# Kernel optimization log

Measured on AMD Instinct MI355X. Metric: run time of the kernel, lower is better.

## Reference

```python
import jax, jax.numpy as jnp
import numpy as np
from jax import lax

B, T, D, H, W = 2, 16, 64, 64, 64
E, HID, K = 4, 128, 3
NS = 0.01  # noise_scale
EPS = 1e-5  # LayerNorm eps (torch default)


def setup_inputs() -> dict:
    key = jax.random.key(0)
    ks = jax.random.split(key, 20)
    r = lambda i, shape, s=1.0: jax.random.normal(ks[i], shape, dtype=jnp.float32) * s
    return {
        "x_real": r(0, (B, T, D, H, W)),
        "x_imag": r(1, (B, T, D, H, W)),
        "dt": jax.random.uniform(ks[2], (B, T), dtype=jnp.float32, minval=0.1, maxval=1.0),
        "noise_eps_real": r(3, (B * H * W, T, D)),
        "noise_eps_imag": r(4, (B * H * W, T, D)),
        "ln_s_w": jnp.ones((2 * D,), jnp.float32),
        "ln_s_b": jnp.zeros((2 * D,), jnp.float32),
        "conv_w": r(5, (K, K, 2 * D, 2 * D), 0.02),  # HWIO
        "conv_b": jnp.zeros((2 * D,), jnp.float32),
        "ln_t_w": jnp.ones((2 * D,), jnp.float32),
        "ln_t_b": jnp.zeros((2 * D,), jnp.float32),
        "lam_re": r(6, (D,)),
        "lam_im": r(7, (D,)),
        "src_bias_re": r(8, (D,), 0.02),
        "src_bias_im": r(9, (D,), 0.02),
        "enc_re": r(10, (D, D), 0.125),
        "enc_im": r(11, (D, D), 0.125),
        "dec_re": r(12, (D, D), 0.125),
        "dec_im": r(13, (D, D), 0.125),
        "router_w": r(14, (2 * D, E), 0.02),
        "router_b": jnp.zeros((E,), jnp.float32),
        "w1": r(15, (E, 2 * D, HID), 0.02),
        "b1": jnp.zeros((E, HID), jnp.float32),
        "w2": r(16, (E, HID, 2 * D), 0.02),
        "b2": jnp.zeros((E, 2 * D), jnp.float32),
    }


def _complex_ln(zr, zi, w, b):
    # LayerNorm over concatenated [real, imag] last dim, then re-split to complex
    zc = jnp.concatenate([zr, zi], axis=-1)
    mu = jnp.mean(zc, -1, keepdims=True)
    var = jnp.var(zc, -1, keepdims=True)
    zn = (zc - mu) * lax.rsqrt(var + EPS) * w + b
    r, i = jnp.split(zn, 2, axis=-1)
    return r + 1j * i


def reference(x_real, x_imag, dt, noise_eps_real, noise_eps_imag,
              ln_s_w, ln_s_b, conv_w, conv_b, ln_t_w, ln_t_b,
              lam_re, lam_im, src_bias_re, src_bias_im,
              enc_re, enc_im, dec_re, dec_im,
              router_w, router_b, w1, b1, w2, b2):
    x = x_real + 1j * x_imag  # (B,T,D,H,W) complex
    resid = x
    # --- spatial: complex norm + clifford-style conv on stacked real/imag channels ---
    xs = jnp.transpose(x.reshape(B * T, D, H, W), (0, 2, 3, 1))  # (BT,H,W,D)
    zn = _complex_ln(xs.real, xs.imag, ln_s_w, ln_s_b)
    xc = jnp.concatenate([zn.real, zn.imag], axis=-1)  # (BT,H,W,2D)
    y = lax.conv_general_dilated(xc, conv_w, (1, 1), 'SAME',
                                 dimension_numbers=('NHWC', 'HWIO', 'NHWC')) + conv_b
    yr, yi = jnp.split(y, 2, axis=-1)
    x = jnp.transpose(yr + 1j * yi, (0, 3, 1, 2)).reshape(B, T, D, H, W) + resid
    resid = x
    # --- temporal: eigen-basis encode, decay-forced parallel scan, decode ---
    xt = jnp.transpose(x, (0, 3, 4, 1, 2)).reshape(B * H * W, T, D)
    xt = _complex_ln(xt.real, xt.imag, ln_t_w, ln_t_b)  # complex (N,T,D)
    dtE = jnp.broadcast_to(dt[:, None, None, :], (B, H, W, T)).reshape(B * H * W, T)
    lam = -jax.nn.softplus(lam_re) + 1j * lam_im  # stable per-mode eigenvalues (D,)
    a = jnp.exp(lam[None, None, :] * dtE[:, :, None])  # decay op (N,T,D)
    forcing = (a - 1.0) / lam  # ZOH forcing op
    Eb = enc_re + 1j * enc_im
    bias = src_bias_re + 1j * src_bias_im
    u = (jnp.einsum('ntd,de->nte', xt, Eb) + bias) * forcing
    u = u + NS * jnp.sqrt(dtE)[:, :, None] * (noise_eps_real + 1j * noise_eps_imag)

    def comb(c1, c2):  # first-order linear recurrence h_t = a_t h_{t-1} + u_t
        a1, b1_ = c1
        a2, b2_ = c2
        return a1 * a2, b1_ * a2 + b2_

    _, h = lax.associative_scan(comb, (a, u), axis=1)
    Db = dec_re + 1j * dec_im
    drift = jnp.einsum('nte,ed->ntd', h, Db).real  # (N,T,D)
    x = jnp.transpose(drift.reshape(B, H, W, T, D), (0, 3, 4, 1, 2)) + resid
    # --- MoE FFN on per-pixel tokens (real/imag concat) ---
    tc = jnp.transpose(x, (0, 1, 3, 4, 2))  # (B,T,H,W,D) complex
    tok = jnp.concatenate([tc.real, tc.imag], axis=-1).reshape(-1, 2 * D)  # (N2,2D)
    gates = jax.nn.softmax(tok @ router_w + router_b, axis=-1)  # (N2,E)
    hdn = jax.nn.gelu(jnp.einsum('nd,edh->neh', tok, w1) + b1)
    yo = jnp.einsum('neh,eho->neo', hdn, w2) + b2
    out = jnp.einsum('ne,neo->no', gates, yo)
    dr, di = jnp.split(out, 2, axis=-1)
    delta = jnp.transpose((dr + 1j * di).reshape(B, T, H, W, D), (0, 1, 4, 2, 3))
    x = x + delta
    return jnp.stack([x.real, x.imag], axis=0)  # (2,B,T,D,H,W)
```

## Files before the change

kernel.cpp:

```cpp
#include <hip/hip_runtime.h>
#include <hip/hip_bf16.h>
#include <math.h>

#define HW 4096
#define TP 264

typedef __attribute__((ext_vector_type(8))) short bf16x8;
typedef _Float16 f16x8 __attribute__((ext_vector_type(8)));
typedef __attribute__((ext_vector_type(4))) float f32x4;

#define MFMA_BF16(a, b, c) __builtin_amdgcn_mfma_f32_16x16x32_bf16((a), (b), (c), 0, 0, 0)
#define MFMA_F16(a, b, c)  __builtin_amdgcn_mfma_f32_16x16x32_f16((a), (b), (c), 0, 0, 0)

__global__ __launch_bounds__(256) void k_prep_t(
    const float* __restrict__ src, __hip_bfloat16* __restrict__ dst)
{
    __shared__ float t[32*33];
    int m  = blockIdx.x;
    int tr = blockIdx.y >> 2, tc = blockIdx.y & 3;
    int tid = threadIdx.x;
    for (int l = tid; l < 1024; l += 256) {
        int r = l >> 5, c = l & 31;
        t[r*33 + c] = src[m*16384 + (tr*32 + r)*128 + (tc*32 + c)];
    }
    __syncthreads();
    for (int l = tid; l < 1024; l += 256) {
        int c = l >> 5, r = l & 31;
        dst[m*16384 + (tc*32 + c)*128 + (tr*32 + r)] = __float2bfloat16(t[r*33 + c]);
    }
}

__global__ __launch_bounds__(256) void k_prep_enc(
    const float* __restrict__ encr, const float* __restrict__ enci,
    const float* __restrict__ decr, const float* __restrict__ deci,
    const float* __restrict__ dt,
    const float* __restrict__ lamr, const float* __restrict__ lami,
    const float* __restrict__ rw,
    _Float16* __restrict__ Benc, _Float16* __restrict__ BdecX,
    float4* __restrict__ coefG, float* __restrict__ nscG,
    __hip_bfloat16* __restrict__ rwB)
{
    int idx = blockIdx.x*256 + threadIdx.x;
    if (idx < 16384) {
        int n = idx >> 7, k = idx & 127;
        int e = n & 63, d = k & 63;
        float v;
        if (n < 64) v = (k < 64) ? encr[d*64 + e] : -enci[d*64 + e];
        else        v = (k < 64) ? enci[d*64 + e] :  encr[d*64 + e];
        Benc[idx] = (_Float16)v;
    }
    if (idx < 16384) {
        int n = idx >> 8, k = idx & 255;
        int kk = k & 127;
        int e = kk & 63;
        float v = (kk < 64) ? decr[e*64 + n] : -deci[e*64 + n];
        BdecX[idx] = (_Float16)v;
    }
    if (idx < 2048) {
        int bt = idx >> 6, e = idx & 63;
        float dtv = dt[bt];
        float lr = lamr[e];
        float sp = (lr > 20.f) ? lr : log1pf(expf(lr));
        float lre = -sp, lim = lami[e];
        float inv = 1.f / (lre*lre + lim*lim);
        float ex = expf(lre*dtv);
        float sn, cs; sincosf(lim*dtv, &sn, &cs);
        float ar = ex*cs, ai = ex*sn;
        float fr = ((ar - 1.f)*lre + ai*lim)*inv;
        float fi = (ai*lre - (ar - 1.f)*lim)*inv;
        coefG[idx] = make_float4(ar, ai, fr, fi);
    }
    if (idx < 2048) {
        int n = idx >> 7, k = idx & 127;
        float v = (n < 4) ? rw[k*4 + n] : 0.f;
        rwB[idx] = __float2bfloat16(v);
    }
    if (idx < 32) nscG[idx] = 0.01f * sqrtf(dt[idx]);
}

__global__ __launch_bounds__(256) void k_ln_s(
    const float* __restrict__ xr, const float* __restrict__ xi,
    const float* __restrict__ lw, const float* __restrict__ lb,
    __hip_bfloat16* __restrict__ out)
{
    __shared__ float tile[64*129];
    __shared__ float ps[64*4];
    __shared__ float ps2[64*4];
    __shared__ float mu_s[64];
    __shared__ float rs_s[64];
    int bt  = blockIdx.x;
    int hw0 = blockIdx.y * 64;
    int tid = threadIdx.x;
    int wl = tid & 63;
    int q  = tid >> 6;
    float s = 0.f, s2 = 0.f;
    for (int c = q; c < 128; c += 4) {
        const float* src = (c < 64) ? xr : xi;
        int d = c & 63;
        float v = src[(bt*64 + d)*HW + hw0 + wl];
        tile[wl*129 + c] = v;
        s += v; s2 += v*v;
    }
    ps[wl*4 + q] = s;
    ps2[wl*4 + q] = s2;
    __syncthreads();
    if (tid < 64) {
        float ss = ps[tid*4+0]+ps[tid*4+1]+ps[tid*4+2]+ps[tid*4+3];
        float qq = ps2[tid*4+0]+ps2[tid*4+1]+ps2[tid*4+2]+ps2[tid*4+3];
        float mu = ss * 0.0078125f;
        float var = qq * 0.0078125f - mu*mu;
        mu_s[tid] = mu;
        rs_s[tid] = rsqrtf(var + 1e-5f);
    }
    __syncthreads();
    int c = tid & 127;
    int r = tid >> 7;
    float wc = lw[c], bc = lb[c];
    for (int wi = r; wi < 64; wi += 2) {
        float v = tile[wi*129 + c];
        out[(size_t)(bt*HW + hw0 + wi)*128 + c] =
            __float2bfloat16((v - mu_s[wi]) * rs_s[wi] * wc + bc);
    }
}

__global__ __launch_bounds__(256) void k_conv_mfma(
    const __hip_bfloat16* __restrict__ xc,
    const __hip_bfloat16* __restrict__ wB,
    const float* __restrict__ cb,
    const float* __restrict__ xr, const float* __restrict__ xi,
    float* __restrict__ x1)
{
    __shared__ __align__(16) short inrow[3*66*136];
    int bt = blockIdx.x, h = blockIdx.y;
    int tid = threadIdx.x;
    if (tid < 96) {
        int r = tid / 32, t2 = tid & 31;
        int px = (t2 & 1) ? 65 : 0;
        int j = t2 >> 1;
        *(float4*)&inrow[(r*66 + px)*136 + j*8] = make_float4(0.f,0.f,0.f,0.f);
    }
    for (int c = tid; c < 3072; c += 256) {
        int r   = c >> 10;
        int rem = c & 1023;
        int px  = rem >> 4;
        int j   = rem & 15;
        int gh  = h + r - 1;
        float4 v = make_float4(0.f,0.f,0.f,0.f);
        if ((unsigned)gh < 64u)
            v = *(const float4*)&xc[(size_t)((bt*HW + gh*64 + px)*128) + j*8];
        *(float4*)&inrow[(r*66 + px + 1)*136 + j*8] = v;
    }
    __syncthreads();

    int wv = tid >> 6, l = tid & 63, lm = l & 15, q = l >> 4;
    int n0 = wv * 32;
    f32x4 acc[4][2];
    #pragma unroll
    for (int mi = 0; mi < 4; mi++)
        #pragma unroll
        for (int ni = 0; ni < 2; ni++)
            acc[mi][ni] = (f32x4){0.f,0.f,0.f,0.f};

    for (int p = 0; p < 9; p++) {
        int kh = p / 3, kw = p - kh*3;
        const __hip_bfloat16* wp = wB + p*16384;
        int abase = (kh*66 + kw)*136;
        #pragma unroll
        for (int ks = 0; ks < 4; ks++) {
            int ko = ks*32 + q*8;
            bf16x8 b0 = *(const bf16x8*)(wp + (n0 + lm)*128 + ko);
            bf16x8 b1 = *(const bf16x8*)(wp + (n0 + 16 + lm)*128 + ko);
            #pragma unroll
            for (int mi = 0; mi < 4; mi++) {
                bf16x8 a = *(const bf16x8*)&inrow[abase + (mi*16 + lm)*136 + ko];
                acc[mi][0] = MFMA_BF16(a, b0, acc[mi][0]);
                acc[mi][1] = MFMA_BF16(a, b1, acc[mi][1]);
            }
        }
    }
    #pragma unroll
    for (int ni = 0; ni < 2; ni++) {
        int oc = n0 + ni*16 + lm;
        float bias = cb[oc];
        const float* rsp = (oc < 64) ? xr : xi;
        const float* rbase = &rsp[(bt*64 + (oc & 63))*HW + h*64];
        #pragma unroll
        for (int mi = 0; mi < 4; mi++) {
            #pragma unroll
            for (int r = 0; r < 4; r++) {
                int w = mi*16 + q*4 + r;
                x1[(size_t)(bt*HW + h*64 + w)*128 + oc] = acc[mi][ni][r] + bias + rbase[w];
            }
        }
    }
}

__global__ __launch_bounds__(128) void k_temporal_mfma(
    float* xio,
    const float* __restrict__ lw, const float* __restrict__ lb,
    const float* __restrict__ sbr, const float* __restrict__ sbi,
    const _Float16* __restrict__ Benc, const _Float16* __restrict__ BdecX,
    const float4* __restrict__ coefG, const float* __restrict__ nscG,
    const float* __restrict__ nzr, const float* __restrict__ nzi)
{
    __shared__ __align__(16) short At[64*TP];
    int n0  = blockIdx.x * 4;
    int b   = n0 >> 12;
    int hw0 = n0 & 4095;
    int tid = threadIdx.x;

    {
        int row = tid >> 1, half = tid & 1;
        int nl = row >> 4, t = row & 15;
        const float4* src = (const float4*)&xio[((size_t)((b*16 + t)*HW) + hw0 + nl)*128 + half*64];
        float4 v[16];
        float s = 0.f, s2 = 0.f;
        #pragma unroll
        for (int j = 0; j < 16; j++) {
            v[j] = src[j];
            s  += v[j].x + v[j].y + v[j].z + v[j].w;
            s2 += v[j].x*v[j].x + v[j].y*v[j].y + v[j].z*v[j].z + v[j].w*v[j].w;
        }
        s  += __shfl_xor(s, 1, 64);
        s2 += __shfl_xor(s2, 1, 64);
        float mu  = s * 0.0078125f;
        float var = s2 * 0.0078125f - mu*mu;
        float rsq = rsqrtf(var + 1e-5f);
        const float4* lw4 = (const float4*)(lw + half*64);
        const float4* lb4 = (const float4*)(lb + half*64);
        short* dstrow = &At[row*TP + half*64];
        #pragma unroll
        for (int j = 0; j < 16; j++) {
            float4 wv4 = lw4[j], bv = lb4[j];
            union { _Float16 h[4]; float2 f; } u;
            u.h[0] = (_Float16)((v[j].x - mu)*rsq*wv4.x + bv.x);
            u.h[1] = (_Float16)((v[j].y - mu)*rsq*wv4.y + bv.y);
            u.h[2] = (_Float16)((v[j].z - mu)*rsq*wv4.z + bv.z);
            u.h[3] = (_Float16)((v[j].w - mu)*rsq*wv4.w + bv.w);
            *(float2*)(dstrow + j*4) = u.f;
        }
    }
    __syncthreads();

    int wv = tid >> 6, l = tid & 63, lm = l & 15, q = l >> 4;

    f32x4 acc[2][8];
    #pragma unroll
    for (int mi = 0; mi < 2; mi++)
        #pragma unroll
        for (int ni = 0; ni < 8; ni++)
            acc[mi][ni] = (f32x4){0.f,0.f,0.f,0.f};
    #pragma unroll
    for (int ks = 0; ks < 4; ks++) {
        int ko = ks*32 + q*8;
        f16x8 a0 = *(const f16x8*)&At[((2*wv+0)*16 + lm)*TP + ko];
        f16x8 a1 = *(const f16x8*)&At[((2*wv+1)*16 + lm)*TP + ko];
        #pragma unroll
        for (int ni = 0; ni < 8; ni++) {
            f16x8 bb = *(const f16x8*)(Benc + (ni*16 + lm)*128 + ko);
            acc[0][ni] = MFMA_F16(a0, bb, acc[0][ni]);
            acc[1][ni] = MFMA_F16(a1, bb, acc[1][ni]);
        }
    }

    int btbase = b*16;
    #pragma unroll
    for (int ni = 0; ni < 4; ni++) {
        int e = ni*16 + lm;
        float br = sbr[e], bi = sbi[e];
        float4 cf[4]; float ns[4];
        #pragma unroll
        for (int r = 0; r < 4; r++) {
            int t = q*4 + r;
            cf[r] = coefG[(btbase + t)*64 + e];
            ns[r] = nscG[btbase + t];
        }
        #pragma unroll
        for (int mi = 0; mi < 2; mi++) {
            int nl = 2*wv + mi;
            int ng = n0 + nl;
            float nrv[4], niv[4];
            #pragma unroll
            for (int r = 0; r < 4; r++) {
                int off = (ng*16 + q*4 + r)*64 + e;
                nrv[r] = nzr[off];
                niv[r] = nzi[off];
            }
            float hr = 0.f, hi = 0.f, Apr = 1.f, Api = 0.f;
            float hrs[4], his[4], Aprs[4], Apis[4];
            #pragma unroll
            for (int r = 0; r < 4; r++) {
                float Sr = acc[mi][ni][r] + br;
                float Si = acc[mi][ni+4][r] + bi;
                float ur = Sr*cf[r].z - Si*cf[r].w + ns[r]*nrv[r];
                float ui = Sr*cf[r].w + Si*cf[r].z + ns[r]*niv[r];
                if (r == 0) { hr = ur; hi = ui; Apr = cf[0].x; Api = cf[0].y; }
                else {
                    float tr = cf[r].x*hr - cf[r].y*hi + ur;
                    float ti = cf[r].x*hi + cf[r].y*hr + ui;
                    hr = tr; hi = ti;
                    tr = cf[r].x*Apr - cf[r].y*Api;
                    ti = cf[r].x*Api + cf[r].y*Apr;
                    Apr = tr; Api = ti;
                }
                hrs[r] = hr; his[r] = hi; Aprs[r] = Apr; Apis[r] = Api;
            }
            float Ar = Apr, Ai = Api, Hr = hr, Hi = hi;
            #pragma unroll
            for (int off = 16; off <= 32; off <<= 1) {
                float pAr = __shfl_up(Ar, off, 64);
                float pAi = __shfl_up(Ai, off, 64);
                float pHr = __shfl_up(Hr, off, 64);
                float pHi = __shfl_up(Hi, off, 64);
                if (l >= off) {
                    Hr = Hr + Ar*pHr - Ai*pHi;
                    Hi = Hi + Ar*pHi + Ai*pHr;
                    float tAr = Ar*pAr - Ai*pAi;
                    float tAi = Ar*pAi + Ai*pAr;
                    Ar = tAr; Ai = tAi;
                }
            }
            float gr = __shfl_up(Hr, 16, 64);
            float gi = __shfl_up(Hi, 16, 64);
            if (q == 0) { gr = 0.f; gi = 0.f; }
            #pragma unroll
            for (int r = 0; r < 4; r++) {
                float fhr = hrs[r] + Aprs[r]*gr - Apis[r]*gi;
                float fhi = his[r] + Aprs[r]*gi + Apis[r]*gr;
                int row = nl*16 + q*4 + r;
                _Float16 hrh = (_Float16)fhr;
                _Float16 hih = (_Float16)fhi;
                *(_Float16*)&At[row*TP + e]        = hrh;
                *(_Float16*)&At[row*TP + 64 + e]   = hih;
                *(_Float16*)&At[row*TP + 128 + e]  = (_Float16)(fhr - (float)hrh);
                *(_Float16*)&At[row*TP + 192 + e]  = (_Float16)(fhi - (float)hih);
            }
        }
    }

    f32x4 acc2[2][4];
    #pragma unroll
    for (int mi = 0; mi < 2; mi++)
        #pragma unroll
        for (int ni = 0; ni < 4; ni++)
            acc2[mi][ni] = (f32x4){0.f,0.f,0.f,0.f};
    #pragma unroll
    for (int ks = 0; ks < 8; ks++) {
        int ko = ks*32 + q*8;
        f16x8 a0 = *(const f16x8*)&At[((2*wv+0)*16 + lm)*TP + ko];
        f16x8 a1 = *(const f16x8*)&At[((2*wv+1)*16 + lm)*TP + ko];
        #pragma unroll
        for (int ni = 0; ni < 4; ni++) {
            f16x8 bb = *(const f16x8*)(BdecX + (ni*16 + lm)*256 + ko);
            acc2[0][ni] = MFMA_F16(a0, bb, acc2[0][ni]);
            acc2[1][ni] = MFMA_F16(a1, bb, acc2[1][ni]);
        }
    }

    #pragma unroll
    for (int mi = 0; mi < 2; mi++) {
        int nl = 2*wv + mi;
        #pragma unroll
        for (int ni = 0; ni < 4; ni++) {
            int d = ni*16 + lm;
            #pragma unroll
            for (int r = 0; r < 4; r++) {
                int t = q*4 + r;
                size_t idx = ((size_t)((b*16 + t)*HW) + hw0 + nl)*128 + d;
                xio[idx] = xio[idx] + acc2[mi][ni][r];
            }
        }
    }
}

__global__ __launch_bounds__(256) void k_moe_mfma(
    const float* __restrict__ xio,
    float* __restrict__ outp,
    const __hip_bfloat16* __restrict__ rwB, const float* __restrict__ rb,
    const __hip_bfloat16* __restrict__ w1b, const float* __restrict__ b1,
    const __hip_bfloat16* __restrict__ w2b, const float* __restrict__ b2)
{
    __shared__ __align__(16) short smem[2*64*136];
    __shared__ float gates[256];
    short* tokA = smem;
    short* hidA = smem + 64*136;
    float* tile = (float*)smem;
    int tok0 = blockIdx.x * 64;
    int tid = threadIdx.x;
    for (int lsd = tid; lsd < 2048; lsd += 256) {
        int t = lsd >> 5, j = lsd & 31;
        float4 v = *(const float4*)&xio[(size_t)(tok0 + t)*128 + j*4];
        union { __hip_bfloat16 h[4]; float2 f; } u;
        u.h[0] = __float2bfloat16(v.x);
        u.h[1] = __float2bfloat16(v.y);
        u.h[2] = __float2bfloat16(v.z);
        u.h[3] = __float2bfloat16(v.w);
        *(float2*)&tokA[t*136 + j*4] = u.f;
    }
    __syncthreads();

    int wv = tid >> 6, l = tid & 63, lm = l & 15, q = l >> 4;
    int n0 = wv * 32;

    {
        f32x4 racc[2];
        racc[0] = (f32x4){0.f,0.f,0.f,0.f};
        racc[1] = (f32x4){0.f,0.f,0.f,0.f};
        #pragma unroll
        for (int ks = 0; ks < 4; ks++) {
            int ko = ks*32 + q*8;
            bf16x8 bb = *(const bf16x8*)(rwB + lm*128 + ko);
            bf16x8 a0 = *(const bf16x8*)&tokA[(n0 + lm)*136 + ko];
            bf16x8 a1 = *(const bf16x8*)&tokA[(n0 + 16 + lm)*136 + ko];
            racc[0] = MFMA_BF16(a0, bb, racc[0]);
            racc[1] = MFMA_BF16(a1, bb, racc[1]);
        }
        float rb_l = rb[lm & 3];
        #pragma unroll
        for (int mi = 0; mi < 2; mi++) {
            #pragma unroll
            for (int r = 0; r < 4; r++) {
                float g = racc[mi][r] + rb_l;
                float mx = fmaxf(g, __shfl_xor(g, 1, 64));
                mx = fmaxf(mx, __shfl_xor(mx, 2, 64));
                float ev = __expf(g - mx);
                float sv = ev + __shfl_xor(ev, 1, 64);
                sv += __shfl_xor(sv, 2, 64);
                if (lm < 4)
                    gates[(n0 + mi*16 + q*4 + r)*4 + lm] = ev * __builtin_amdgcn_rcpf(sv);
            }
        }
    }

    f32x4 outa[4][2];
    #pragma unroll
    for (int mi = 0; mi < 4; mi++)
        #pragma unroll
        for (int ni = 0; ni < 2; ni++)
            outa[mi][ni] = (f32x4){0.f,0.f,0.f,0.f};

    for (int e = 0; e < 4; e++) {
        f32x4 acc1[4][2];
        #pragma unroll
        for (int mi = 0; mi < 4; mi++)
            #pragma unroll
            for (int ni = 0; ni < 2; ni++)
                acc1[mi][ni] = (f32x4){0.f,0.f,0.f,0.f};
        const __hip_bfloat16* wp1 = w1b + e*16384;
        #pragma unroll
        for (int ks = 0; ks < 4; ks++) {
            int ko = ks*32 + q*8;
            bf16x8 b0  = *(const bf16x8*)(wp1 + (n0 + lm)*128 + ko);
            bf16x8 b1v = *(const bf16x8*)(wp1 + (n0 + 16 + lm)*128 + ko);
            #pragma unroll
            for (int mi = 0; mi < 4; mi++) {
                bf16x8 a = *(const bf16x8*)&tokA[(mi*16 + lm)*136 + ko];
                acc1[mi][0] = MFMA_BF16(a, b0,  acc1[mi][0]);
                acc1[mi][1] = MFMA_BF16(a, b1v, acc1[mi][1]);
            }
        }
        __syncthreads();
        #pragma unroll
        for (int ni = 0; ni < 2; ni++) {
            int hcol = n0 + ni*16 + lm;
            float bb = b1[e*128 + hcol];
            #pragma unroll
            for (int mi = 0; mi < 4; mi++) {
                #pragma unroll
                for (int r = 0; r < 4; r++) {
                    float xv = acc1[mi][ni][r] + bb;
                    float x2 = xv*xv;
                    float t2 = xv*(1.5957691216057308f + 0.07135481627260025f*x2);
                    float ee = __expf(t2);
                    float hv = xv*(1.f - __builtin_amdgcn_rcpf(ee + 1.f));
                    int m = mi*16 + q*4 + r;
                    *(__hip_bfloat16*)&hidA[m*136 + hcol] = __float2bfloat16(hv);
                }
            }
        }
        __syncthreads();
        f32x4 acc2[4][2];
        #pragma unroll
        for (int mi = 0; mi < 4; mi++)
            #pragma unroll
            for (int ni = 0; ni < 2; ni++)
                acc2[mi][ni] = (f32x4){0.f,0.f,0.f,0.f};
        const __hip_bfloat16* wp2 = w2b + e*16384;
        #pragma unroll
        for (int ks = 0; ks < 4; ks++) {
            int ko = ks*32 + q*8;
            bf16x8 b0  = *(const bf16x8*)(wp2 + (n0 + lm)*128 + ko);
            bf16x8 b1v = *(const bf16x8*)(wp2 + (n0 + 16 + lm)*128 + ko);
            #pragma unroll
            for (int mi = 0; mi < 4; mi++) {
                bf16x8 a = *(const bf16x8*)&hidA[(mi*16 + lm)*136 + ko];
                acc2[mi][0] = MFMA_BF16(a, b0,  acc2[mi][0]);
                acc2[mi][1] = MFMA_BF16(a, b1v, acc2[mi][1]);
            }
        }
        #pragma unroll
        for (int ni = 0; ni < 2; ni++) {
            int ocol = n0 + ni*16 + lm;
            float bb = b2[e*128 + ocol];
            #pragma unroll
            for (int mi = 0; mi < 4; mi++) {
                #pragma unroll
                for (int r = 0; r < 4; r++) {
                    int m = mi*16 + q*4 + r;
                    float g = gates[m*4 + e];
                    outa[mi][ni][r] += g * (acc2[mi][ni][r] + bb);
                }
            }
        }
        __syncthreads();
    }
    #pragma unroll
    for (int ni = 0; ni < 2; ni++) {
        int col = n0 + ni*16 + lm;
        #pragma unroll
        for (int mi = 0; mi < 4; mi++) {
            #pragma unroll
            for (int r = 0; r < 4; r++) {
                int m = mi*16 + q*4 + r;
                tile[m*129 + col] = xio[(size_t)(tok0 + m)*128 + col] + outa[mi][ni][r];
            }
        }
    }
    __syncthreads();
    int bt = tok0 >> 12;
    int hw0 = tok0 & 4095;
    for (int lid = tid; lid < 8192; lid += 256) {
        int c = lid >> 6, m = lid & 63;
        int p = c >> 6, d = c & 63;
        outp[((size_t)((p*32 + bt)*64 + d))*HW + hw0 + m] = tile[m*129 + c];
    }
}

extern "C" void kernel_launch(void* const* d_in, const int* in_sizes, int n_in,
                              void* d_out, int out_size, void* d_ws, size_t ws_size,
                              hipStream_t stream)
{
    const float* x_real = (const float*)d_in[0];
    const float* x_imag = (const float*)d_in[1];
    const float* dt     = (const float*)d_in[2];
    const float* nzr    = (const float*)d_in[3];
    const float* nzi    = (const float*)d_in[4];
    const float* ln_s_w = (const float*)d_in[5];
    const float* ln_s_b = (const float*)d_in[6];
    const float* conv_w = (const float*)d_in[7];
    const float* conv_b = (const float*)d_in[8];
    const float* ln_t_w = (const float*)d_in[9];
    const float* ln_t_b = (const float*)d_in[10];
    const float* lam_re = (const float*)d_in[11];
    const float* lam_im = (const float*)d_in[12];
    const float* sbr    = (const float*)d_in[13];
    const float* sbi    = (const float*)d_in[14];
    const float* enc_re = (const float*)d_in[15];
    const float* enc_im = (const float*)d_in[16];
    const float* dec_re = (const float*)d_in[17];
    const float* dec_im = (const float*)d_in[18];
    const float* rw     = (const float*)d_in[19];
    const float* rb     = (const float*)d_in[20];
    const float* w1     = (const float*)d_in[21];
    const float* b1     = (const float*)d_in[22];
    const float* w2     = (const float*)d_in[23];
    const float* b2     = (const float*)d_in[24];

    char* ws = (char*)d_ws;
    float* bufA = (float*)ws;
    __hip_bfloat16* bufB = (__hip_bfloat16*)(ws + (size_t)64*1024*1024);
    __hip_bfloat16* wBc  = (__hip_bfloat16*)(ws + (size_t)96*1024*1024);
    __hip_bfloat16* w1b  = wBc + 9*16384;
    __hip_bfloat16* w2b  = w1b + 4*16384;
    _Float16* Benc  = (_Float16*)(w2b + 4*16384);
    _Float16* BdecX = Benc + 16384;
    float4* coefG = (float4*)(BdecX + 16384);
    float* nscG   = (float*)(coefG + 2048);
    __hip_bfloat16* rwB = (__hip_bfloat16*)(nscG + 32);
    float* outp = (float*)d_out;

    k_prep_t  <<<dim3(9,16), 256, 0, stream>>>(conv_w, wBc);
    k_prep_t  <<<dim3(4,16), 256, 0, stream>>>(w1, w1b);
    k_prep_t  <<<dim3(4,16), 256, 0, stream>>>(w2, w2b);
    k_prep_enc<<<64,         256, 0, stream>>>(enc_re, enc_im, dec_re, dec_im,
                                               dt, lam_re, lam_im, rw,
                                               Benc, BdecX, coefG, nscG, rwB);

    k_ln_s         <<<dim3(32,64), 256, 0, stream>>>(x_real, x_imag, ln_s_w, ln_s_b, bufB);
    k_conv_mfma    <<<dim3(32,64), 256, 0, stream>>>(bufB, wBc, conv_b, x_real, x_imag, bufA);
    k_temporal_mfma<<<2048,        128, 0, stream>>>(bufA, ln_t_w, ln_t_b, sbr, sbi,
                                                     Benc, BdecX, coefG, nscG, nzr, nzi);
    k_moe_mfma     <<<2048,        256, 0, stream>>>(bufA, outp, rwB, rb, w1b, b1, w2b, b2);
}
```

Before: 505.0 us.

## Double-buffer MoE hidden tile and overlap next expert's GEMM1 with GEMM2

The MoE kernel now uses two hidden-activation buffers in shared memory. It computes expert e+1's first GEMM and GELU while expert e's second GEMM runs, which drops from three block barriers per expert to one. It also XOR-swizzles the hidden tile columns to reduce LDS bank conflicts on the A-operand reads. The cost is more shared memory (an extra 17KB), which can lower occupancy, plus higher register pressure from keeping both accumulator sets live.

```diff
diff --git a/kernel.cpp b/kernel.cpp
--- a/kernel.cpp
+++ b/kernel.cpp
@@ -11,6 +11,13 @@
 
 #define MFMA_BF16(a, b, c) __builtin_amdgcn_mfma_f32_16x16x32_bf16((a), (b), (c), 0, 0, 0)
 #define MFMA_F16(a, b, c)  __builtin_amdgcn_mfma_f32_16x16x32_f16((a), (b), (c), 0, 0, 0)
+
+static __device__ __forceinline__ float gelu_f(float xv) {
+    float x2 = xv*xv;
+    float t2 = xv*(1.5957691216057308f + 0.07135481627260025f*x2);
+    float ee = __expf(t2);
+    return xv*(1.f - __builtin_amdgcn_rcpf(ee + 1.f));
+}
 
 __global__ __launch_bounds__(256) void k_prep_t(
     const float* __restrict__ src, __hip_bfloat16* __restrict__ dst)
@@ -380,10 +387,11 @@
     const __hip_bfloat16* __restrict__ w1b, const float* __restrict__ b1,
     const __hip_bfloat16* __restrict__ w2b, const float* __restrict__ b2)
 {
-    __shared__ __align__(16) short smem[2*64*136];
+    __shared__ __align__(16) short smem[3*64*136];
     __shared__ float gates[256];
     short* tokA = smem;
-    short* hidA = smem + 64*136;
+    short* hid0 = smem + 64*136;
+    short* hid1 = smem + 2*64*136;
     float* tile = (float*)smem;
     int tok0 = blockIdx.x * 64;
     int tid = threadIdx.x;
@@ -439,14 +447,14 @@
         for (int ni = 0; ni < 2; ni++)
             outa[mi][ni] = (f32x4){0.f,0.f,0.f,0.f};
 
-    for (int e = 0; e < 4; e++) {
+    {
         f32x4 acc1[4][2];
         #pragma unroll
         for (int mi = 0; mi < 4; mi++)
             #pragma unroll
             for (int ni = 0; ni < 2; ni++)
                 acc1[mi][ni] = (f32x4){0.f,0.f,0.f,0.f};
-        const __hip_bfloat16* wp1 = w1b + e*16384;
+        const __hip_bfloat16* wp1 = w1b;
         #pragma unroll
         for (int ks = 0; ks < 4; ks++) {
             int ko = ks*32 + q*8;
@@ -459,26 +467,26 @@
                 acc1[mi][1] = MFMA_BF16(a, b1v, acc1[mi][1]);
             }
         }
-        __syncthreads();
         #pragma unroll
         for (int ni = 0; ni < 2; ni++) {
             int hcol = n0 + ni*16 + lm;
-            float bb = b1[e*128 + hcol];
+            float bb = b1[hcol];
             #pragma unroll
             for (int mi = 0; mi < 4; mi++) {
                 #pragma unroll
                 for (int r = 0; r < 4; r++) {
-                    float xv = acc1[mi][ni][r] + bb;
-                    float x2 = xv*xv;
-                    float t2 = xv*(1.5957691216057308f + 0.07135481627260025f*x2);
-                    float ee = __expf(t2);
-                    float hv = xv*(1.f - __builtin_amdgcn_rcpf(ee + 1.f));
+                    float hv = gelu_f(acc1[mi][ni][r] + bb);
                     int m = mi*16 + q*4 + r;
-                    *(__hip_bfloat16*)&hidA[m*136 + hcol] = __float2bfloat16(hv);
+                    *(__hip_bfloat16*)&hid0[m*136 + (hcol ^ ((m&7)<<3))] = __float2bfloat16(hv);
                 }
             }
         }
-        __syncthreads();
+    }
+    __syncthreads();
+
+    #pragma unroll
+    for (int e = 0; e < 4; e++) {
+        const short* hb = (e & 1) ? hid1 : hid0;
         f32x4 acc2[4][2];
         #pragma unroll
         for (int mi = 0; mi < 4; mi++)
@@ -491,9 +499,10 @@
             int ko = ks*32 + q*8;
             bf16x8 b0  = *(const bf16x8*)(wp2 + (n0 + lm)*128 + ko);
             bf16x8 b1v = *(const bf16x8*)(wp2 + (n0 + 16 + lm)*128 + ko);
+            int sko = ko ^ ((lm&7)<<3);
             #pragma unroll
             for (int mi = 0; mi < 4; mi++) {
-                bf16x8 a = *(const bf16x8*)&hidA[(mi*16 + lm)*136 + ko];
+                bf16x8 a = *(const bf16x8*)&hb[(mi*16 + lm)*136 + sko];
                 acc2[mi][0] = MFMA_BF16(a, b0,  acc2[mi][0]);
                 acc2[mi][1] = MFMA_BF16(a, b1v, acc2[mi][1]);
             }
@@ -512,8 +521,45 @@
                 }
             }
         }
+        if (e < 3) {
+            short* hn = (e & 1) ? hid0 : hid1;
+            f32x4 acc1[4][2];
+            #pragma unroll
+            for (int mi = 0; mi < 4; mi++)
+                #pragma unroll
+                for (int ni = 0; ni < 2; ni++)
+                    acc1[mi][ni] = (f32x4){0.f,0.f,0.f,0.f};
+            const __hip_bfloat16* wp1 = w1b + (e+1)*16384;
+            #pragma unroll
+            for (int ks = 0; ks < 4; ks++) {
+                int ko = ks*32 + q*8;
+                bf16x8 b0  = *(const bf16x8*)(wp1 + (n0 + lm)*128 + ko);
+                bf16x8 b1v = *(const bf16x8*)(wp1 + (n0 + 16 + lm)*128 + ko);
+                #pragma unroll
+                for (int mi = 0; mi < 4; mi++) {
+                    bf16x8 a = *(const bf16x8*)&tokA[(mi*16 + lm)*136 + ko];
+                    acc1[mi][0] = MFMA_BF16(a, b0,  acc1[mi][0]);
+                    acc1[mi][1] = MFMA_BF16(a, b1v, acc1[mi][1]);
+                }
+            }
+            #pragma unroll
+            for (int ni = 0; ni < 2; ni++) {
+                int hcol = n0 + ni*16 + lm;
+                float bb = b1[(e+1)*128 + hcol];
+                #pragma unroll
+                for (int mi = 0; mi < 4; mi++) {
+                    #pragma unroll
+                    for (int r = 0; r < 4; r++) {
+                        float hv = gelu_f(acc1[mi][ni][r] + bb);
+                        int m = mi*16 + q*4 + r;
+                        *(__hip_bfloat16*)&hn[m*136 + (hcol ^ ((m&7)<<3))] = __float2bfloat16(hv);
+                    }
+                }
+            }
+        }
         __syncthreads();
     }
+
     #pragma unroll
     for (int ni = 0; ni < 2; ni++) {
         int col = n0 + ni*16 + lm;
```

After: 529.9 us. +4.9%, slower.

## Split MoE FFN work across waves by token rows to drop expert-loop barriers

Applied to the files above, without the earlier changes.

The MoE FFN kernel now gives each wave 16 token rows across all 128 output columns, instead of 32 columns across all 64 rows. Each wave then writes and reads only its own rows of the hidden buffer and gate values. That lets the per-expert __syncthreads calls be removed and the expert loop be fully unrolled. In exchange, each wave loads every weight column fragment from global memory, which is four times the weight-fragment traffic per wave. Register pressure from the fully unrolled loop may also rise.

```diff
diff --git a/kernel.cpp b/kernel.cpp
--- a/kernel.cpp
+++ b/kernel.cpp
@@ -11,6 +11,13 @@
 
 #define MFMA_BF16(a, b, c) __builtin_amdgcn_mfma_f32_16x16x32_bf16((a), (b), (c), 0, 0, 0)
 #define MFMA_F16(a, b, c)  __builtin_amdgcn_mfma_f32_16x16x32_f16((a), (b), (c), 0, 0, 0)
+
+static __device__ __forceinline__ float gelu_f(float xv) {
+    float x2 = xv*xv;
+    float t2 = xv*(1.5957691216057308f + 0.07135481627260025f*x2);
+    float ee = __expf(t2);
+    return xv*(1.f - __builtin_amdgcn_rcpf(ee + 1.f));
+}
 
 __global__ __launch_bounds__(256) void k_prep_t(
     const float* __restrict__ src, __hip_bfloat16* __restrict__ dst)
@@ -400,130 +407,100 @@
     __syncthreads();
 
     int wv = tid >> 6, l = tid & 63, lm = l & 15, q = l >> 4;
-    int n0 = wv * 32;
+    int r0 = wv * 16;
 
     {
-        f32x4 racc[2];
-        racc[0] = (f32x4){0.f,0.f,0.f,0.f};
-        racc[1] = (f32x4){0.f,0.f,0.f,0.f};
+        f32x4 racc = (f32x4){0.f,0.f,0.f,0.f};
         #pragma unroll
         for (int ks = 0; ks < 4; ks++) {
             int ko = ks*32 + q*8;
             bf16x8 bb = *(const bf16x8*)(rwB + lm*128 + ko);
-            bf16x8 a0 = *(const bf16x8*)&tokA[(n0 + lm)*136 + ko];
-            bf16x8 a1 = *(const bf16x8*)&tokA[(n0 + 16 + lm)*136 + ko];
-            racc[0] = MFMA_BF16(a0, bb, racc[0]);
-            racc[1] = MFMA_BF16(a1, bb, racc[1]);
+            bf16x8 a  = *(const bf16x8*)&tokA[(r0 + lm)*136 + ko];
+            racc = MFMA_BF16(a, bb, racc);
         }
         float rb_l = rb[lm & 3];
         #pragma unroll
-        for (int mi = 0; mi < 2; mi++) {
-            #pragma unroll
-            for (int r = 0; r < 4; r++) {
-                float g = racc[mi][r] + rb_l;
-                float mx = fmaxf(g, __shfl_xor(g, 1, 64));
-                mx = fmaxf(mx, __shfl_xor(mx, 2, 64));
-                float ev = __expf(g - mx);
-                float sv = ev + __shfl_xor(ev, 1, 64);
-                sv += __shfl_xor(sv, 2, 64);
-                if (lm < 4)
-                    gates[(n0 + mi*16 + q*4 + r)*4 + lm] = ev * __builtin_amdgcn_rcpf(sv);
-            }
-        }
-    }
-
-    f32x4 outa[4][2];
-    #pragma unroll
-    for (int mi = 0; mi < 4; mi++)
-        #pragma unroll
-        for (int ni = 0; ni < 2; ni++)
-            outa[mi][ni] = (f32x4){0.f,0.f,0.f,0.f};
-
+        for (int r = 0; r < 4; r++) {
+            float g = racc[r] + rb_l;
+            float mx = fmaxf(g, __shfl_xor(g, 1, 64));
+            mx = fmaxf(mx, __shfl_xor(mx, 2, 64));
+            float ev = __expf(g - mx);
+            float sv = ev + __shfl_xor(ev, 1, 64);
+            sv += __shfl_xor(sv, 2, 64);
+            if (lm < 4)
+                gates[(r0 + q*4 + r)*4 + lm] = ev * __builtin_amdgcn_rcpf(sv);
+        }
+    }
+
+    f32x4 outa[8];
+    #pragma unroll
+    for (int ni = 0; ni < 8; ni++)
+        outa[ni] = (f32x4){0.f,0.f,0.f,0.f};
+
+    #pragma unroll
     for (int e = 0; e < 4; e++) {
-        f32x4 acc1[4][2];
-        #pragma unroll
-        for (int mi = 0; mi < 4; mi++)
-            #pragma unroll
-            for (int ni = 0; ni < 2; ni++)
-                acc1[mi][ni] = (f32x4){0.f,0.f,0.f,0.f};
+        f32x4 acc1[8];
+        #pragma unroll
+        for (int ni = 0; ni < 8; ni++)
+            acc1[ni] = (f32x4){0.f,0.f,0.f,0.f};
         const __hip_bfloat16* wp1 = w1b + e*16384;
         #pragma unroll
         for (int ks = 0; ks < 4; ks++) {
             int ko = ks*32 + q*8;
-            bf16x8 b0  = *(const bf16x8*)(wp1 + (n0 + lm)*128 + ko);
-            bf16x8 b1v = *(const bf16x8*)(wp1 + (n0 + 16 + lm)*128 + ko);
-            #pragma unroll
-            for (int mi = 0; mi < 4; mi++) {
-                bf16x8 a = *(const bf16x8*)&tokA[(mi*16 + lm)*136 + ko];
-                acc1[mi][0] = MFMA_BF16(a, b0,  acc1[mi][0]);
-                acc1[mi][1] = MFMA_BF16(a, b1v, acc1[mi][1]);
-            }
-        }
-        __syncthreads();
-        #pragma unroll
-        for (int ni = 0; ni < 2; ni++) {
-            int hcol = n0 + ni*16 + lm;
+            bf16x8 a = *(const bf16x8*)&tokA[(r0 + lm)*136 + ko];
+            #pragma unroll
+            for (int ni = 0; ni < 8; ni++) {
+                bf16x8 bb = *(const bf16x8*)(wp1 + (ni*16 + lm)*128 + ko);
+                acc1[ni] = MFMA_BF16(a, bb, acc1[ni]);
+            }
+        }
+        #pragma unroll
+        for (int ni = 0; ni < 8; ni++) {
+            int hcol = ni*16 + lm;
             float bb = b1[e*128 + hcol];
             #pragma unroll
-            for (int mi = 0; mi < 4; mi++) {
-                #pragma unroll
-                for (int r = 0; r < 4; r++) {
-                    float xv = acc1[mi][ni][r] + bb;
-                    float x2 = xv*xv;
-                    float t2 = xv*(1.5957691216057308f + 0.07135481627260025f*x2);
-                    float ee = __expf(t2);
-                    float hv = xv*(1.f - __builtin_amdgcn_rcpf(ee + 1.f));
-                    int m = mi*16 + q*4 + r;
-                    *(__hip_bfloat16*)&hidA[m*136 + hcol] = __float2bfloat16(hv);
-                }
-            }
-        }
-        __syncthreads();
-        f32x4 acc2[4][2];
-        #pragma unroll
-        for (int mi = 0; mi < 4; mi++)
-            #pragma unroll
-            for (int ni = 0; ni < 2; ni++)
-                acc2[mi][ni] = (f32x4){0.f,0.f,0.f,0.f};
+            for (int r = 0; r < 4; r++) {
+                float hv = gelu_f(acc1[ni][r] + bb);
+                int m = r0 + q*4 + r;
+                *(__hip_bfloat16*)&hidA[m*136 + hcol] = __float2bfloat16(hv);
+            }
+        }
+        f32x4 acc2[8];
+        #pragma unroll
+        for (int ni = 0; ni < 8; ni++)
+            acc2[ni] = (f32x4){0.f,0.f,0.f,0.f};
         const __hip_bfloat16* wp2 = w2b + e*16384;
         #pragma unroll
         for (int ks = 0; ks < 4; ks++) {
             int ko = ks*32 + q*8;
-            bf16x8 b0  = *(const bf16x8*)(wp2 + (n0 + lm)*128 + ko);
-            bf16x8 b1v = *(const bf16x8*)(wp2 + (n0 + 16 + lm)*128 + ko);
-            #pragma unroll
-            for (int mi = 0; mi < 4; mi++) {
-                bf16x8 a = *(const bf16x8*)&hidA[(mi*16 + lm)*136 + ko];
-                acc2[mi][0] = MFMA_BF16(a, b0,  acc2[mi][0]);
-                acc2[mi][1] = MFMA_BF16(a, b1v, acc2[mi][1]);
-            }
-        }
-        #pragma unroll
-        for (int ni = 0; ni < 2; ni++) {
-            int ocol = n0 + ni*16 + lm;
-            float bb = b2[e*128 + ocol];
-            #pragma unroll
-            for (int mi = 0; mi < 4; mi++) {
-                #pragma unroll
-                for (int r = 0; r < 4; r++) {
-                    int m = mi*16 + q*4 + r;
-                    float g = gates[m*4 + e];
-                    outa[mi][ni][r] += g * (acc2[mi][ni][r] + bb);
-                }
-            }
-        }
-        __syncthreads();
-    }
-    #pragma unroll
-    for (int ni = 0; ni < 2; ni++) {
-        int col = n0 + ni*16 + lm;
-        #pragma unroll
-        for (int mi = 0; mi < 4; mi++) {
-            #pragma unroll
-            for (int r = 0; r < 4; r++) {
-                int m = mi*16 + q*4 + r;
-                tile[m*129 + col] = xio[(size_t)(tok0 + m)*128 + col] + outa[mi][ni][r];
-            }
+            bf16x8 a = *(const bf16x8*)&hidA[(r0 + lm)*136 + ko];
+            #pragma unroll
+            for (int ni = 0; ni < 8; ni++) {
+                bf16x8 bb = *(const bf16x8*)(wp2 + (ni*16 + lm)*128 + ko);
+                acc2[ni] = MFMA_BF16(a, bb, acc2[ni]);
+            }
+        }
+        float g4[4];
+        #pragma unroll
+        for (int r = 0; r < 4; r++)
+            g4[r] = gates[(r0 + q*4 + r)*4 + e];
+        #pragma unroll
+        for (int ni = 0; ni < 8; ni++) {
+            float bb = b2[e*128 + ni*16 + lm];
+            #pragma unroll
+            for (int r = 0; r < 4; r++)
+                outa[ni][r] += g4[r] * (acc2[ni][r] + bb);
+        }
+    }
+    __syncthreads();
+
+    #pragma unroll
+    for (int ni = 0; ni < 8; ni++) {
+        int col = ni*16 + lm;
+        #pragma unroll
+        for (int r = 0; r < 4; r++) {
+            int m = r0 + q*4 + r;
+            tile[m*129 + col] = xio[(size_t)(tok0 + m)*128 + col] + outa[ni][r];
         }
     }
     __syncthreads();
```

Result: slower. 710.0 us (+40.6%).
